# Kernel tuning notes

Hardware: AMD Instinct MI355X
Metric: run time of the kernel (lower is better)

Reference implementation:

```python
import jax, jax.numpy as jnp
import numpy as np

N = 50000   # nodes
E = 800000  # edges (avg degree 16)
H = 128     # hidden_channels
G = 50      # num_gaussians
CUT = 6.0   # cutoff
PI = float(np.pi)
SHIFT = float(np.log(2.0))


def ssp(x):
    # ShiftedSoftplus
    return jax.nn.softplus(x) - SHIFT


def setup_inputs() -> dict:
    key = jax.random.key(0)
    ks = jax.random.split(key, 32)
    p = lambda k, shape: jax.random.normal(k, shape, jnp.float32) * 0.05
    inp = {
        "z": jax.random.normal(ks[0], (N, 3), jnp.float32),
        "dist": jax.random.uniform(ks[1], (E,), jnp.float32) * CUT,
        "edge_index": jax.random.randint(ks[2], (2, E), 0, N, dtype=jnp.int32),
        "init_w": p(ks[3], (3, H)), "init_b": jnp.zeros((H,), jnp.float32),
        # layer 0
        "e0_lin_w": p(ks[4], (H, H)),
        "e0_m0_w": p(ks[5], (G, H)), "e0_m0_b": jnp.zeros((H,), jnp.float32),
        "e0_m2_w": p(ks[6], (H, H)), "e0_m2_b": jnp.zeros((H,), jnp.float32),
        "v0_l1_w": p(ks[7], (H, H)), "v0_l1_b": jnp.zeros((H,), jnp.float32),
        "v0_l2_w": p(ks[8], (H, H)), "v0_l2_b": jnp.zeros((H,), jnp.float32),
        # layer 1
        "e1_lin_w": p(ks[9], (H, H)),
        "e1_m0_w": p(ks[10], (G, H)), "e1_m0_b": jnp.zeros((H,), jnp.float32),
        "e1_m2_w": p(ks[11], (H, H)), "e1_m2_b": jnp.zeros((H,), jnp.float32),
        "v1_l1_w": p(ks[12], (H, H)), "v1_l1_b": jnp.zeros((H,), jnp.float32),
        "v1_l2_w": p(ks[13], (H, H)), "v1_l2_b": jnp.zeros((H,), jnp.float32),
        # readout
        "u_l1_w": p(ks[14], (H, H)), "u_l1_b": jnp.zeros((H,), jnp.float32),
        "u_l2_w": p(ks[15], (H, 3)), "u_l2_b": jnp.zeros((3,), jnp.float32),
    }
    return inp


def reference(z, dist, edge_index, init_w, init_b,
              e0_lin_w, e0_m0_w, e0_m0_b, e0_m2_w, e0_m2_b,
              v0_l1_w, v0_l1_b, v0_l2_w, v0_l2_b,
              e1_lin_w, e1_m0_w, e1_m0_b, e1_m2_w, e1_m2_b,
              v1_l1_w, v1_l1_b, v1_l2_w, v1_l2_b,
              u_l1_w, u_l1_b, u_l2_w, u_l2_b):
    n = z.shape[0]
    j, i = edge_index[0], edge_index[1]  # source, target

    # RBF embedding of dist.to(long)  (torch truncates toward zero)
    offset = jnp.linspace(0.0, CUT, G, dtype=jnp.float32)
    coeff = -0.5 / (offset[1] - offset[0]) ** 2
    demb = jnp.exp(coeff * (jnp.trunc(dist)[:, None] - offset[None, :]) ** 2)  # [E,G]

    # cosine cutoff gate
    C = 0.5 * (jnp.cos(dist * (PI / CUT)) + 1.0)  # [E]

    v = z @ init_w + init_b  # [N,H]

    layers = [
        (e0_lin_w, e0_m0_w, e0_m0_b, e0_m2_w, e0_m2_b, v0_l1_w, v0_l1_b, v0_l2_w, v0_l2_b),
        (e1_lin_w, e1_m0_w, e1_m0_b, e1_m2_w, e1_m2_b, v1_l1_w, v1_l1_b, v1_l2_w, v1_l2_b),
    ]
    for lin_w, m0_w, m0_b, m2_w, m2_b, l1_w, l1_b, l2_w, l2_b in layers:
        # update_e: filter MLP on RBF, gated by cutoff, times gathered node feats
        W = (ssp(demb @ m0_w + m0_b) @ m2_w + m2_b) * C[:, None]  # [E,H]
        e = (v @ lin_w)[j] * W                                     # [E,H]
        # update_v: scatter-add into target nodes, then node MLP + residual
        agg = jax.ops.segment_sum(e, i, num_segments=n)            # [N,H]
        v = v + (ssp(agg @ l1_w + l1_b) @ l2_w + l2_b)

    # update_u readout
    return ssp(v @ u_l1_w + u_l1_b) @ u_l2_w + u_l2_b  # [N,3]
```

## Files before the change

kernel.cpp:

```cpp
#include <hip/hip_runtime.h>
#include <cstdint>
#include <cstddef>

#define HD 128
#define GD 50
static constexpr float PI_F   = 3.14159265358979323846f;
static constexpr float CUTF   = 6.0f;
static constexpr float SHIFTF = 0.69314718055994530942f;

typedef _Float16 f16x8 __attribute__((ext_vector_type(8)));
typedef _Float16 f16x2 __attribute__((ext_vector_type(2)));
typedef float    f32x4 __attribute__((ext_vector_type(4)));

struct Ptr8 { const float* p[8]; };

__device__ __forceinline__ float ssp(float x) {
    float e = __expf(-fabsf(x));
    return fmaxf(x, 0.0f) + __logf(1.0f + e) - SHIFTF;
}

__device__ __forceinline__ _Float16* t16(_Float16* base, int row, int byte) {
    return (_Float16*)((char*)base + row * 256 + (byte ^ ((row & 7) << 4)));
}

__device__ __forceinline__ void mfma_ct(const f16x8 af[4],
                                        const _Float16* __restrict__ Bf,
                                        int lane, f32x4 acc[2], int ctb) {
    #pragma unroll
    for (int ks = 0; ks < 4; ++ks)
        #pragma unroll
        for (int c = 0; c < 2; ++c)
            acc[c] = __builtin_amdgcn_mfma_f32_16x16x32_f16(
                af[ks], ((const f16x8*)Bf)[((ctb + c) * 4 + ks) * 64 + lane],
                acc[c], 0, 0, 0);
}

template <int ACT>
__device__ __forceinline__ void acc_to_t16_ct(const f32x4 acc[2], const float* bias,
                                              int lane, _Float16* tile, int ctb) {
    int col0 = lane & 15, r0 = (lane >> 4) * 4;
    #pragma unroll
    for (int c = 0; c < 2; ++c) {
        int cc = (ctb + c) * 16 + col0;
        float bs = bias ? bias[cc] : 0.f;
        #pragma unroll
        for (int r = 0; r < 4; ++r) {
            float o = acc[c][r] + bs;
            if (ACT) o = ssp(o);
            *t16(tile, r0 + r, cc * 2) = (_Float16)o;
        }
    }
}

__device__ __forceinline__ void t16_to_af(_Float16* tile, int lane, f16x8 af[4]) {
    int row = lane & 15, kgB = (lane >> 4) * 16;
    #pragma unroll
    for (int ks = 0; ks < 4; ++ks)
        af[ks] = *(const f16x8*)t16(tile, row, ks * 64 + kgB);
}

__device__ __forceinline__ void vz_ct(const float* __restrict__ z,
                                      const float* __restrict__ iw,
                                      const float* __restrict__ ib,
                                      int rowbase, int lane, int n, int ctb,
                                      f32x4 vz[2]) {
    int col0 = lane & 15, r0 = (lane >> 4) * 4;
    float zr[4][3];
    #pragma unroll
    for (int r = 0; r < 4; ++r) {
        int row = min(rowbase + r0 + r, n - 1);
        zr[r][0] = z[row * 3 + 0];
        zr[r][1] = z[row * 3 + 1];
        zr[r][2] = z[row * 3 + 2];
    }
    #pragma unroll
    for (int c = 0; c < 2; ++c) {
        int cc = (ctb + c) * 16 + col0;
        float w0 = iw[cc], w1 = iw[HD + cc], w2 = iw[2 * HD + cc], bz = ib[cc];
        #pragma unroll
        for (int r = 0; r < 4; ++r)
            vz[c][r] = fmaf(zr[r][0], w0, fmaf(zr[r][1], w1, fmaf(zr[r][2], w2, bz)));
    }
}

__global__ __launch_bounds__(HD) void k_wtab2(Ptr8 P, float* __restrict__ wtab) {
    const int bin = blockIdx.x, layer = blockIdx.y;
    const int t = threadIdx.x;
    const float* m0w = P.p[layer * 4 + 0];
    const float* m0b = P.p[layer * 4 + 1];
    const float* m2w = P.p[layer * 4 + 2];
    const float* m2b = P.p[layer * 4 + 3];
    __shared__ float hbuf[HD];

    const float spacing = CUTF / (GD - 1);
    const float coeff   = -0.5f / (spacing * spacing);

    float acc = m0b[t];
    #pragma unroll 5
    for (int g = 0; g < GD; ++g) {
        float d = (float)bin - (float)g * spacing;
        acc = fmaf(__expf(coeff * d * d), m0w[g * HD + t], acc);
    }
    hbuf[t] = ssp(acc);
    __syncthreads();

    float acc2 = m2b[t];
    #pragma unroll 8
    for (int k = 0; k < HD; ++k)
        acc2 = fmaf(hbuf[k], m2w[k * HD + t], acc2);
    wtab[(layer * 7 + bin) * HD + t] = acc2;
}

__global__ __launch_bounds__(256) void k_prepB7(Ptr8 P, _Float16* __restrict__ Bf,
                                                int* __restrict__ deg, int n) {
    int slot = blockIdx.y;
    int idx = blockIdx.x * 256 + threadIdx.x;
    if (slot == 7) {
        for (int i = idx; i < n; i += 2048) deg[i] = 0;
        return;
    }
    if (idx >= 2048) return;
    const float* W = P.p[slot];
    int l  = idx & 63;
    int f  = idx >> 6;
    int ks = f & 3, ct = f >> 2;
    int col = ct * 16 + (l & 15);
    int k0  = ks * 32 + ((l >> 4) << 3);
    f16x8 o;
    #pragma unroll
    for (int j = 0; j < 8; ++j) o[j] = (_Float16)W[(size_t)(k0 + j) * HD + col];
    ((f16x8*)(Bf + (size_t)slot * 16384))[idx] = o;
}

__global__ __launch_bounds__(256) void k_deg(const int* __restrict__ ei,
                                             int* __restrict__ deg, int nedges) {
    int e = blockIdx.x * 256 + threadIdx.x;
    if (e < nedges) atomicAdd(&deg[ei[nedges + e]], 1);
}

__global__ __launch_bounds__(1024) void k_scan1(const int* __restrict__ deg,
                                                int* __restrict__ rowstart,
                                                int* __restrict__ blocksum, int n) {
    __shared__ int wsum[16];
    int tid  = threadIdx.x;
    int lane = tid & 63, wid = tid >> 6;
    int i = blockIdx.x * 1024 + tid;
    int val = (i < n) ? deg[i] : 0;
    int x = val;
    #pragma unroll
    for (int off = 1; off < 64; off <<= 1) {
        int y = __shfl_up(x, off, 64);
        if (lane >= off) x += y;
    }
    if (lane == 63) wsum[wid] = x;
    __syncthreads();
    if (wid == 0) {
        int s = (lane < 16) ? wsum[lane] : 0;
        #pragma unroll
        for (int off = 1; off < 16; off <<= 1) {
            int y = __shfl_up(s, off, 64);
            if (lane >= off) s += y;
        }
        if (lane < 16) wsum[lane] = s;
    }
    __syncthreads();
    int wbase = (wid > 0) ? wsum[wid - 1] : 0;
    if (i <= n) rowstart[i] = wbase + x - val;
    if (tid == 1023) blocksum[blockIdx.x] = wsum[15];
}

__global__ __launch_bounds__(64) void k_scan2(int* __restrict__ blocksum, int nb) {
    int lane = threadIdx.x;
    int v = (lane < nb) ? blocksum[lane] : 0;
    int x = v;
    #pragma unroll
    for (int off = 1; off < 64; off <<= 1) {
        int y = __shfl_up(x, off, 64);
        if (lane >= off) x += y;
    }
    if (lane < nb) blocksum[lane] = x - v;
}

__global__ __launch_bounds__(1024) void k_scan3(int* __restrict__ rowstart,
                                                int* __restrict__ cursor,
                                                const int* __restrict__ blocksum,
                                                int n) {
    int i = blockIdx.x * 1024 + threadIdx.x;
    if (i <= n) {
        int rs = rowstart[i] + blocksum[blockIdx.x];
        rowstart[i] = rs;
        if (i < n) cursor[i] = rs;
    }
}

__global__ __launch_bounds__(256) void k_fused_fe(const int* __restrict__ ei,
                                                  const float* __restrict__ dist,
                                                  int* __restrict__ cursor,
                                                  int2* __restrict__ ecomb,
                                                  int nedges, int escGrid,
                                                  const float* __restrict__ z,
                                                  const float* __restrict__ iw,
                                                  const float* __restrict__ ib,
                                                  const _Float16* __restrict__ BfL,
                                                  _Float16* __restrict__ vlin_h,
                                                  int n) {
    __shared__ __attribute__((aligned(16))) _Float16 tile16[2048];
    int bx = blockIdx.x;
    if (bx < escGrid) {
        int base = bx * 1024 + (int)threadIdx.x;
        #pragma unroll
        for (int k = 0; k < 4; ++k) {
            int e = base + k * 256;
            if (e < nedges) {
                int   j = ei[e];
                int   i = ei[nedges + e];
                float d = dist[e];
                int bin = min((int)d, 6);
                float Cg = 0.5f * (cosf(d * (PI_F / CUTF)) + 1.0f);
                int pos = atomicAdd(&cursor[i], 1);
                ecomb[pos] = make_int2(j | (bin << 25), __float_as_int(Cg));
            }
        }
        return;
    }
    int tid = threadIdx.x, lane = tid & 63, wid = tid >> 6;
    int rowbase = (bx - escGrid) * 16;
    int arow = min(rowbase + (lane & 15), n - 1);
    float z0 = z[arow * 3 + 0], z1 = z[arow * 3 + 1], z2 = z[arow * 3 + 2];
    int kg = (lane >> 4) * 8;

    f16x8 af[4];
    #pragma unroll
    for (int ks = 0; ks < 4; ++ks) {
        f16x8 h;
        #pragma unroll
        for (int j = 0; j < 8; ++j) {
            int c = ks * 32 + kg + j;
            h[j] = (_Float16)fmaf(z0, iw[c], fmaf(z1, iw[HD + c], fmaf(z2, iw[2 * HD + c], ib[c])));
        }
        af[ks] = h;
    }

    f32x4 acc[2];
    acc[0] = (f32x4){0.f, 0.f, 0.f, 0.f};
    acc[1] = (f32x4){0.f, 0.f, 0.f, 0.f};
    mfma_ct(af, BfL, lane, acc, wid * 2);
    acc_to_t16_ct<0>(acc, nullptr, lane, tile16, wid * 2);
    __syncthreads();
    int row = tid >> 4, g8 = tid & 15;
    if (rowbase + row < n)
        ((f16x8*)vlin_h)[(size_t)(rowbase + row) * 16 + g8] =
            *(const f16x8*)t16(tile16, row, g8 * 16);
}

__global__ __launch_bounds__(256) void k_agg(const int* __restrict__ rowstart,
                                             const int2* __restrict__ ecomb,
                                             const _Float16* __restrict__ vlin_h,
                                             const float* __restrict__ wtab,
                                             _Float16* __restrict__ agg_h, int n) {
    __shared__ float lwt[7 * HD];
    int tid = threadIdx.x;
    if (tid < 224) ((float4*)lwt)[tid] = ((const float4*)wtab)[tid];
    __syncthreads();

    int node = blockIdx.x * 4 + (tid >> 6);
    if (node >= n) return;
    int lane = tid & 63;
    int beg = rowstart[node], end = rowstart[node + 1];

    float accx = 0.f, accy = 0.f;
    const float* lwt2 = lwt + 2 * lane;
    int e = beg;
    for (; e + 3 < end; e += 4) {
        int2 c0 = ecomb[e],     c1 = ecomb[e + 1];
        int2 c2 = ecomb[e + 2], c3 = ecomb[e + 3];
        f16x2 h0 = *(const f16x2*)(vlin_h + (size_t)(c0.x & 0x01FFFFFF) * HD + 2 * lane);
        f16x2 h1 = *(const f16x2*)(vlin_h + (size_t)(c1.x & 0x01FFFFFF) * HD + 2 * lane);
        f16x2 h2 = *(const f16x2*)(vlin_h + (size_t)(c2.x & 0x01FFFFFF) * HD + 2 * lane);
        f16x2 h3 = *(const f16x2*)(vlin_h + (size_t)(c3.x & 0x01FFFFFF) * HD + 2 * lane);
        float2 w0 = *(const float2*)(lwt2 + (c0.x >> 25) * HD);
        float2 w1 = *(const float2*)(lwt2 + (c1.x >> 25) * HD);
        float2 w2 = *(const float2*)(lwt2 + (c2.x >> 25) * HD);
        float2 w3 = *(const float2*)(lwt2 + (c3.x >> 25) * HD);
        float g0 = __int_as_float(c0.y), g1 = __int_as_float(c1.y);
        float g2 = __int_as_float(c2.y), g3 = __int_as_float(c3.y);
        accx = fmaf((float)h0[0], w0.x * g0, accx);
        accy = fmaf((float)h0[1], w0.y * g0, accy);
        accx = fmaf((float)h1[0], w1.x * g1, accx);
        accy = fmaf((float)h1[1], w1.y * g1, accy);
        accx = fmaf((float)h2[0], w2.x * g2, accx);
        accy = fmaf((float)h2[1], w2.y * g2, accy);
        accx = fmaf((float)h3[0], w3.x * g3, accx);
        accy = fmaf((float)h3[1], w3.y * g3, accy);
    }
    for (; e < end; ++e) {
        int2 c0 = ecomb[e];
        f16x2 h0 = *(const f16x2*)(vlin_h + (size_t)(c0.x & 0x01FFFFFF) * HD + 2 * lane);
        float2 w0 = *(const float2*)(lwt2 + (c0.x >> 25) * HD);
        float g0 = __int_as_float(c0.y);
        accx = fmaf((float)h0[0], w0.x * g0, accx);
        accy = fmaf((float)h0[1], w0.y * g0, accy);
    }
    f16x2 o; o[0] = (_Float16)accx; o[1] = (_Float16)accy;
    *(f16x2*)(agg_h + (size_t)node * HD + 2 * lane) = o;
}

__global__ __launch_bounds__(256) void k_mid(const _Float16* __restrict__ agg_h,
                                             const _Float16* __restrict__ Bf1,
                                             const float* __restrict__ b1,
                                             const _Float16* __restrict__ Bf2,
                                             const float* __restrict__ b2,
                                             const _Float16* __restrict__ BfL,
                                             const float* __restrict__ z,
                                             const float* __restrict__ iw,
                                             const float* __restrict__ ib,
                                             f32x4* __restrict__ vres4,
                                             _Float16* __restrict__ vlin_h, int n) {
    __shared__ __attribute__((aligned(16))) _Float16 tile16[2048];
    int tid = threadIdx.x, lane = tid & 63, wid = tid >> 6;
    int rowbase = blockIdx.x * 16;
    int ctb = wid * 2;

    int arow = min(rowbase + (lane & 15), n - 1);
    int kg = (lane >> 4) * 8;
    f16x8 af[4];
    #pragma unroll
    for (int ks = 0; ks < 4; ++ks)
        af[ks] = *(const f16x8*)(agg_h + (size_t)arow * HD + ks * 32 + kg);

    f32x4 acc[2];
    acc[0] = (f32x4){0.f, 0.f, 0.f, 0.f};
    acc[1] = (f32x4){0.f, 0.f, 0.f, 0.f};
    mfma_ct(af, Bf1, lane, acc, ctb);
    acc_to_t16_ct<1>(acc, b1, lane, tile16, ctb);
    __syncthreads();
    t16_to_af(tile16, lane, af);
    __syncthreads();

    acc[0] = (f32x4){0.f, 0.f, 0.f, 0.f};
    acc[1] = (f32x4){0.f, 0.f, 0.f, 0.f};
    mfma_ct(af, Bf2, lane, acc, ctb);

    f32x4 vz[2];
    vz_ct(z, iw, ib, rowbase, lane, n, ctb, vz);
    int col0 = lane & 15;
    #pragma unroll
    for (int c = 0; c < 2; ++c) {
        float bs = b2[(ctb + c) * 16 + col0];
        #pragma unroll
        for (int r = 0; r < 4; ++r) acc[c][r] += bs + vz[c][r];
        vres4[((size_t)blockIdx.x * 8 + ctb + c) * 64 + lane] = acc[c];
    }

    acc_to_t16_ct<0>(acc, nullptr, lane, tile16, ctb);
    __syncthreads();
    t16_to_af(tile16, lane, af);
    __syncthreads();

    acc[0] = (f32x4){0.f, 0.f, 0.f, 0.f};
    acc[1] = (f32x4){0.f, 0.f, 0.f, 0.f};
    mfma_ct(af, BfL, lane, acc, ctb);
    acc_to_t16_ct<0>(acc, nullptr, lane, tile16, ctb);
    __syncthreads();
    int row = tid >> 4, g8 = tid & 15;
    if (rowbase + row < n)
        ((f16x8*)vlin_h)[(size_t)(rowbase + row) * 16 + g8] =
            *(const f16x8*)t16(tile16, row, g8 * 16);
}

__global__ __launch_bounds__(256) void k_back(const _Float16* __restrict__ agg_h,
                                              const _Float16* __restrict__ Bf1,
                                              const float* __restrict__ b1,
                                              const _Float16* __restrict__ Bf2,
                                              const float* __restrict__ b2,
                                              const _Float16* __restrict__ BfU,
                                              const float* __restrict__ ub1,
                                              const float* __restrict__ w2,
                                              const float* __restrict__ ub2,
                                              const f32x4* __restrict__ vres4,
                                              float* __restrict__ out, int n) {
    __shared__ __attribute__((aligned(16))) _Float16 tile16[2048];
    __shared__ float red[4][16][3];
    int tid = threadIdx.x, lane = tid & 63, wid = tid >> 6;
    int rowbase = blockIdx.x * 16;
    int ctb = wid * 2;

    int arow = min(rowbase + (lane & 15), n - 1);
    int kg = (lane >> 4) * 8;
    f16x8 af[4];
    #pragma unroll
    for (int ks = 0; ks < 4; ++ks)
        af[ks] = *(const f16x8*)(agg_h + (size_t)arow * HD + ks * 32 + kg);

    f32x4 acc[2];
    acc[0] = (f32x4){0.f, 0.f, 0.f, 0.f};
    acc[1] = (f32x4){0.f, 0.f, 0.f, 0.f};
    mfma_ct(af, Bf1, lane, acc, ctb);
    acc_to_t16_ct<1>(acc, b1, lane, tile16, ctb);
    __syncthreads();
    t16_to_af(tile16, lane, af);
    __syncthreads();

    acc[0] = (f32x4){0.f, 0.f, 0.f, 0.f};
    acc[1] = (f32x4){0.f, 0.f, 0.f, 0.f};
    mfma_ct(af, Bf2, lane, acc, ctb);

    int col0 = lane & 15;
    #pragma unroll
    for (int c = 0; c < 2; ++c) {
        float bs = b2[(ctb + c) * 16 + col0];
        f32x4 rv = vres4[((size_t)blockIdx.x * 8 + ctb + c) * 64 + lane];
        #pragma unroll
        for (int r = 0; r < 4; ++r) acc[c][r] += bs + rv[r];
    }

    acc_to_t16_ct<0>(acc, nullptr, lane, tile16, ctb);
    __syncthreads();
    t16_to_af(tile16, lane, af);

    acc[0] = (f32x4){0.f, 0.f, 0.f, 0.f};
    acc[1] = (f32x4){0.f, 0.f, 0.f, 0.f};
    mfma_ct(af, BfU, lane, acc, ctb);

    int r0 = (lane >> 4) * 4;
    float p0[4] = {0.f, 0.f, 0.f, 0.f};
    float p1[4] = {0.f, 0.f, 0.f, 0.f};
    float p2[4] = {0.f, 0.f, 0.f, 0.f};
    #pragma unroll
    for (int c = 0; c < 2; ++c) {
        int cc = (ctb + c) * 16 + col0;
        float bu = ub1[cc];
        float w20 = w2[cc * 3 + 0], w21 = w2[cc * 3 + 1], w22 = w2[cc * 3 + 2];
        #pragma unroll
        for (int r = 0; r < 4; ++r) {
            float u = ssp(acc[c][r] + bu);
            p0[r] = fmaf(u, w20, p0[r]);
            p1[r] = fmaf(u, w21, p1[r]);
            p2[r] = fmaf(u, w22, p2[r]);
        }
    }
    #pragma unroll
    for (int m = 1; m < 16; m <<= 1) {
        #pragma unroll
        for (int r = 0; r < 4; ++r) {
            p0[r] += __shfl_xor(p0[r], m, 64);
            p1[r] += __shfl_xor(p1[r], m, 64);
            p2[r] += __shfl_xor(p2[r], m, 64);
        }
    }
    if (col0 == 0) {
        #pragma unroll
        for (int r = 0; r < 4; ++r) {
            red[wid][r0 + r][0] = p0[r];
            red[wid][r0 + r][1] = p1[r];
            red[wid][r0 + r][2] = p2[r];
        }
    }
    __syncthreads();
    if (tid < 48) {
        int row = tid / 3, c = tid % 3;
        float s = red[0][row][c] + red[1][row][c] + red[2][row][c] + red[3][row][c];
        if (rowbase + row < n)
            out[(size_t)(rowbase + row) * 3 + c] = s + ub2[c];
    }
}

extern "C" void kernel_launch(void* const* d_in, const int* in_sizes, int n_in,
                              void* d_out, int out_size, void* d_ws, size_t ws_size,
                              hipStream_t stream) {
    const float* z      = (const float*)d_in[0];
    const float* dist   = (const float*)d_in[1];
    const int*   ei     = (const int*)d_in[2];
    const float* init_w = (const float*)d_in[3];
    const float* init_b = (const float*)d_in[4];

    const float* L[2][9];
    for (int l = 0; l < 2; ++l)
        for (int p = 0; p < 9; ++p)
            L[l][p] = (const float*)d_in[5 + l * 9 + p];

    const float* u_l1_w = (const float*)d_in[23];
    const float* u_l1_b = (const float*)d_in[24];
    const float* u_l2_w = (const float*)d_in[25];
    const float* u_l2_b = (const float*)d_in[26];
    float* out = (float*)d_out;

    const int N = in_sizes[0] / 3;
    const int E = in_sizes[1];

    const int nb16     = (N + 15) / 16;
    const int escGrid  = (E + 1023) / 1024;
    const int edgeGrid = (E + 255) / 256;
    const int scanB    = (N + 1 + 1023) / 1024;
    const int aggGrid  = (N + 3) / 4;

    float* wtab   = (float*)d_ws;
    float* bf     = wtab + 2048;
    float* vres   = bf + 57344;
    float* vh     = vres + (size_t)nb16 * 2048;
    float* aggh   = vh + (size_t)N * 64;
    int2*  ecomb  = (int2*)(aggh + (size_t)N * 64);
    int*   deg    = (int*)(ecomb + E);
    int*   rowstart = deg + N;
    int*   cursor = rowstart + N + 1;
    int*   blocksum = cursor + N;

    _Float16* vlin_h = (_Float16*)vh;
    _Float16* agg_h  = (_Float16*)aggh;
    f32x4*    vres4  = (f32x4*)vres;
    _Float16* Bf     = (_Float16*)bf;
    _Float16* BfW[7];
    for (int i = 0; i < 7; ++i) BfW[i] = Bf + (size_t)i * 16384;

    Ptr8 wt; wt.p[0] = L[0][1]; wt.p[1] = L[0][2]; wt.p[2] = L[0][3]; wt.p[3] = L[0][4];
             wt.p[4] = L[1][1]; wt.p[5] = L[1][2]; wt.p[6] = L[1][3]; wt.p[7] = L[1][4];
    k_wtab2<<<dim3(7, 2), HD, 0, stream>>>(wt, wtab);

    Ptr8 pb; pb.p[0] = L[0][0]; pb.p[1] = L[0][5]; pb.p[2] = L[0][7];
             pb.p[3] = L[1][0]; pb.p[4] = L[1][5]; pb.p[5] = L[1][7];
             pb.p[6] = u_l1_w;  pb.p[7] = u_l1_w;
    k_prepB7<<<dim3(8, 8), 256, 0, stream>>>(pb, Bf, deg, N);

    k_deg<<<edgeGrid, 256, 0, stream>>>(ei, deg, E);
    k_scan1<<<scanB, 1024, 0, stream>>>(deg, rowstart, blocksum, N);
    k_scan2<<<1, 64, 0, stream>>>(blocksum, scanB);
    k_scan3<<<scanB, 1024, 0, stream>>>(rowstart, cursor, blocksum, N);

    k_fused_fe<<<escGrid + nb16, 256, 0, stream>>>(ei, dist, cursor, ecomb, E, escGrid,
                                                   z, init_w, init_b, BfW[0], vlin_h, N);

    k_agg<<<aggGrid, 256, 0, stream>>>(rowstart, ecomb, vlin_h, wtab, agg_h, N);
    k_mid<<<nb16, 256, 0, stream>>>(agg_h, BfW[1], L[0][6], BfW[2], L[0][8],
                                    BfW[3], z, init_w, init_b, vres4, vlin_h, N);
    k_agg<<<aggGrid, 256, 0, stream>>>(rowstart, ecomb, vlin_h, wtab + 7 * HD, agg_h, N);
    k_back<<<nb16, 256, 0, stream>>>(agg_h, BfW[4], L[1][6], BfW[5], L[1][8],
                                     BfW[6], u_l1_b, u_l2_w, u_l2_b, vres4, out, N);
}
```

Baseline: 356.4 us.

## Split edge CSR fill into atomic-position and write passes, deepen aggregation unroll

The fused edge-scatter/front kernel becomes three kernels. The first pass batches 8 atomics per thread and records each edge's CSR position. The second pass does the scattered ecomb writes using those positions. A standalone front kernel computes the initial node projection. Aggregation now issues 8 independent gathers per iteration to raise memory-level parallelism, at the cost of extra launches, an extra pos array round-trip, and lost overlap between the edge fill and the node GEMM.

```diff
diff --git a/kernel.cpp b/kernel.cpp
--- a/kernel.cpp
+++ b/kernel.cpp
@@ -193,38 +193,51 @@
     }
 }
 
-__global__ __launch_bounds__(256) void k_fused_fe(const int* __restrict__ ei,
-                                                  const float* __restrict__ dist,
-                                                  int* __restrict__ cursor,
-                                                  int2* __restrict__ ecomb,
-                                                  int nedges, int escGrid,
-                                                  const float* __restrict__ z,
-                                                  const float* __restrict__ iw,
-                                                  const float* __restrict__ ib,
-                                                  const _Float16* __restrict__ BfL,
-                                                  _Float16* __restrict__ vlin_h,
-                                                  int n) {
+__global__ __launch_bounds__(256) void k_epos(const int* __restrict__ ei,
+                                              int* __restrict__ cursor,
+                                              int* __restrict__ pos,
+                                              int nedges) {
+    int base = blockIdx.x * 2048 + threadIdx.x;
+    int p[8];
+    #pragma unroll
+    for (int k = 0; k < 8; ++k) {
+        int e = base + k * 256;
+        if (e < nedges) p[k] = atomicAdd(&cursor[ei[nedges + e]], 1);
+    }
+    #pragma unroll
+    for (int k = 0; k < 8; ++k) {
+        int e = base + k * 256;
+        if (e < nedges) pos[e] = p[k];
+    }
+}
+
+__global__ __launch_bounds__(256) void k_ewrite(const int* __restrict__ ei,
+                                                const float* __restrict__ dist,
+                                                const int* __restrict__ pos,
+                                                int2* __restrict__ ecomb,
+                                                int nedges) {
+    int base = blockIdx.x * 2048 + threadIdx.x;
+    #pragma unroll
+    for (int k = 0; k < 8; ++k) {
+        int e = base + k * 256;
+        if (e < nedges) {
+            int   j = ei[e];
+            float d = dist[e];
+            int bin = min((int)d, 6);
+            float Cg = 0.5f * (cosf(d * (PI_F / CUTF)) + 1.0f);
+            ecomb[pos[e]] = make_int2(j | (bin << 25), __float_as_int(Cg));
+        }
+    }
+}
+
+__global__ __launch_bounds__(256) void k_front(const float* __restrict__ z,
+                                               const float* __restrict__ iw,
+                                               const float* __restrict__ ib,
+                                               const _Float16* __restrict__ BfL,
+                                               _Float16* __restrict__ vlin_h, int n) {
     __shared__ __attribute__((aligned(16))) _Float16 tile16[2048];
-    int bx = blockIdx.x;
-    if (bx < escGrid) {
-        int base = bx * 1024 + (int)threadIdx.x;
-        #pragma unroll
-        for (int k = 0; k < 4; ++k) {
-            int e = base + k * 256;
-            if (e < nedges) {
-                int   j = ei[e];
-                int   i = ei[nedges + e];
-                float d = dist[e];
-                int bin = min((int)d, 6);
-                float Cg = 0.5f * (cosf(d * (PI_F / CUTF)) + 1.0f);
-                int pos = atomicAdd(&cursor[i], 1);
-                ecomb[pos] = make_int2(j | (bin << 25), __float_as_int(Cg));
-            }
-        }
-        return;
-    }
     int tid = threadIdx.x, lane = tid & 63, wid = tid >> 6;
-    int rowbase = (bx - escGrid) * 16;
+    int rowbase = blockIdx.x * 16;
     int arow = min(rowbase + (lane & 15), n - 1);
     float z0 = z[arow * 3 + 0], z1 = z[arow * 3 + 1], z2 = z[arow * 3 + 2];
     int kg = (lane >> 4) * 8;
@@ -271,27 +284,37 @@
     float accx = 0.f, accy = 0.f;
     const float* lwt2 = lwt + 2 * lane;
     int e = beg;
+    for (; e + 7 < end; e += 8) {
+        int2 cc[8];
+        #pragma unroll
+        for (int k = 0; k < 8; ++k) cc[k] = ecomb[e + k];
+        f16x2 hh[8];
+        #pragma unroll
+        for (int k = 0; k < 8; ++k)
+            hh[k] = *(const f16x2*)(vlin_h + (size_t)(cc[k].x & 0x01FFFFFF) * HD + 2 * lane);
+        float2 ww[8];
+        #pragma unroll
+        for (int k = 0; k < 8; ++k)
+            ww[k] = *(const float2*)(lwt2 + (cc[k].x >> 25) * HD);
+        #pragma unroll
+        for (int k = 0; k < 8; ++k) {
+            float g = __int_as_float(cc[k].y);
+            accx = fmaf((float)hh[k][0], ww[k].x * g, accx);
+            accy = fmaf((float)hh[k][1], ww[k].y * g, accy);
+        }
+    }
     for (; e + 3 < end; e += 4) {
-        int2 c0 = ecomb[e],     c1 = ecomb[e + 1];
-        int2 c2 = ecomb[e + 2], c3 = ecomb[e + 3];
-        f16x2 h0 = *(const f16x2*)(vlin_h + (size_t)(c0.x & 0x01FFFFFF) * HD + 2 * lane);
-        f16x2 h1 = *(const f16x2*)(vlin_h + (size_t)(c1.x & 0x01FFFFFF) * HD + 2 * lane);
-        f16x2 h2 = *(const f16x2*)(vlin_h + (size_t)(c2.x & 0x01FFFFFF) * HD + 2 * lane);
-        f16x2 h3 = *(const f16x2*)(vlin_h + (size_t)(c3.x & 0x01FFFFFF) * HD + 2 * lane);
-        float2 w0 = *(const float2*)(lwt2 + (c0.x >> 25) * HD);
-        float2 w1 = *(const float2*)(lwt2 + (c1.x >> 25) * HD);
-        float2 w2 = *(const float2*)(lwt2 + (c2.x >> 25) * HD);
-        float2 w3 = *(const float2*)(lwt2 + (c3.x >> 25) * HD);
-        float g0 = __int_as_float(c0.y), g1 = __int_as_float(c1.y);
-        float g2 = __int_as_float(c2.y), g3 = __int_as_float(c3.y);
-        accx = fmaf((float)h0[0], w0.x * g0, accx);
-        accy = fmaf((float)h0[1], w0.y * g0, accy);
-        accx = fmaf((float)h1[0], w1.x * g1, accx);
-        accy = fmaf((float)h1[1], w1.y * g1, accy);
-        accx = fmaf((float)h2[0], w2.x * g2, accx);
-        accy = fmaf((float)h2[1], w2.y * g2, accy);
-        accx = fmaf((float)h3[0], w3.x * g3, accx);
-        accy = fmaf((float)h3[1], w3.y * g3, accy);
+        int2 cc[4];
+        #pragma unroll
+        for (int k = 0; k < 4; ++k) cc[k] = ecomb[e + k];
+        #pragma unroll
+        for (int k = 0; k < 4; ++k) {
+            f16x2 h = *(const f16x2*)(vlin_h + (size_t)(cc[k].x & 0x01FFFFFF) * HD + 2 * lane);
+            float2 w = *(const float2*)(lwt2 + (cc[k].x >> 25) * HD);
+            float g = __int_as_float(cc[k].y);
+            accx = fmaf((float)h[0], w.x * g, accx);
+            accy = fmaf((float)h[1], w.y * g, accy);
+        }
     }
     for (; e < end; ++e) {
         int2 c0 = ecomb[e];
@@ -489,7 +512,7 @@
     const int E = in_sizes[1];
 
     const int nb16     = (N + 15) / 16;
-    const int escGrid  = (E + 1023) / 1024;
+    const int e8Grid   = (E + 2047) / 2048;
     const int edgeGrid = (E + 255) / 256;
     const int scanB    = (N + 1 + 1023) / 1024;
     const int aggGrid  = (N + 3) / 4;
@@ -500,7 +523,8 @@
     float* vh     = vres + (size_t)nb16 * 2048;
     float* aggh   = vh + (size_t)N * 64;
     int2*  ecomb  = (int2*)(aggh + (size_t)N * 64);
-    int*   deg    = (int*)(ecomb + E);
+    int*   pos    = (int*)(ecomb + E);
+    int*   deg    = pos + E;
     int*   rowstart = deg + N;
     int*   cursor = rowstart + N + 1;
     int*   blocksum = cursor + N;
@@ -525,10 +549,10 @@
     k_scan1<<<scanB, 1024, 0, stream>>>(deg, rowstart, blocksum, N);
     k_scan2<<<1, 64, 0, stream>>>(blocksum, scanB);
     k_scan3<<<scanB, 1024, 0, stream>>>(rowstart, cursor, blocksum, N);
-
-    k_fused_fe<<<escGrid + nb16, 256, 0, stream>>>(ei, dist, cursor, ecomb, E, escGrid,
-                                                   z, init_w, init_b, BfW[0], vlin_h, N);
-
+    k_epos<<<e8Grid, 256, 0, stream>>>(ei, cursor, pos, E);
+    k_ewrite<<<e8Grid, 256, 0, stream>>>(ei, dist, pos, ecomb, E);
+
+    k_front<<<nb16, 256, 0, stream>>>(z, init_w, init_b, BfW[0], vlin_h, N);
     k_agg<<<aggGrid, 256, 0, stream>>>(rowstart, ecomb, vlin_h, wtab, agg_h, N);
     k_mid<<<nb16, 256, 0, stream>>>(agg_h, BfW[1], L[0][6], BfW[2], L[0][8],
                                     BfW[3], z, init_w, init_b, vres4, vlin_h, N);
```

Result: no change. 350.3 us (-1.7%).
